# Kernel optimization log

Hardware: AMD Instinct MI355X
Metric: run time of the kernel (lower is better)

The kernel has to match this reference:

```python
import jax, jax.numpy as jnp
import numpy as np

TOKEN_DIM = 4
EPS = 1e-6


def setup_inputs() -> dict:
    key = jax.random.key(0)
    k_x, k_w = jax.random.split(key)
    B, S, E = 8, 8192, 512
    EMB = 512
    x = jax.random.normal(k_x, (B, S, E), dtype=jnp.float32)
    ln_gamma = jnp.ones((E,), dtype=jnp.float32)
    ln_beta = jnp.zeros((E,), dtype=jnp.float32)
    # glorot-ish scale for the compression kernel [token_dim*E, EMB]
    W = jax.random.normal(k_w, (TOKEN_DIM * E, EMB), dtype=jnp.float32) * 0.02
    b = jnp.zeros((EMB,), dtype=jnp.float32)
    return {"x": x, "ln_gamma": ln_gamma, "ln_beta": ln_beta, "W": W, "b": b}


def reference(x, ln_gamma, ln_beta, W, b):
    B, S, E = x.shape
    # LayerNormalization over the feature axis (center + scale)
    mean = jnp.mean(x, axis=-1, keepdims=True)
    var = jnp.mean(jnp.square(x - mean), axis=-1, keepdims=True)
    h = (x - mean) * jax.lax.rsqrt(var + EPS) * ln_gamma + ln_beta
    # Divide: split sequence axis by token_dim and merge factor into feature axis
    # [B, S, E] -> [B, S//T, T*E]
    h = h.reshape(B, S // TOKEN_DIM, TOKEN_DIM * E)
    # Dense compression + exact gelu (keras 'gelu' uses erf form)
    out = jnp.einsum('bsf,fd->bsd', h, W) + b
    return jax.nn.gelu(out, approximate=False)
```

## Files before the change

### kernel.cpp

```cpp
#include <hip/hip_runtime.h>
#include <hip/hip_bf16.h>
#include <cstdint>

#define XROWS   65536
#define E       512
#define MROWS   16384
#define KDIM    2048
#define NDIM    512
#define NT      32

typedef __attribute__((ext_vector_type(4))) float f32x4;
typedef __attribute__((ext_vector_type(8))) unsigned short u16x8;
typedef __attribute__((ext_vector_type(8))) __bf16 bf16x8;

__device__ __forceinline__ unsigned short f2bf(float f) {
  unsigned u = __builtin_bit_cast(unsigned, f);
  u += 0x7FFFu + ((u >> 16) & 1u);
  return (unsigned short)(u >> 16);
}

typedef const __attribute__((address_space(1))) unsigned char ga_u8;
typedef __attribute__((address_space(3))) unsigned char ls_u8;
__device__ __forceinline__ void gload16(const void* g, void* l) {
  __builtin_amdgcn_global_load_lds((ga_u8*)g, (ls_u8*)l, 16, 0, 0);
}

__device__ __forceinline__ float gelu_f(float v) {
  float p = v * (2.3022083f + 0.1029432f * (v * v));
  p = fminf(p, 80.0f);
  const float Ee = exp2f(p);
  return v * Ee * __builtin_amdgcn_rcpf(Ee + 1.0f);
}

__global__ __launch_bounds__(256) void wt_kernel(const float* __restrict__ W,
                                                 const float* __restrict__ gamma,
                                                 unsigned short* __restrict__ WT) {
  __shared__ float tile[64][68];
  const int t  = threadIdx.x;
  const int bk = blockIdx.x >> 3;
  const int bn = blockIdx.x & 7;
  const int c4 = (t & 15) * 4;
#pragma unroll
  for (int i = 0; i < 4; ++i) {
    const int r = (t >> 4) + i * 16;
    const f32x4 v = *(const f32x4*)&W[(size_t)(bk * 64 + r) * NDIM + bn * 64 + c4];
    tile[r][c4 + 0] = v.x; tile[r][c4 + 1] = v.y;
    tile[r][c4 + 2] = v.z; tile[r][c4 + 3] = v.w;
  }
  __syncthreads();
#pragma unroll
  for (int j = 0; j < 2; ++j) {
    const int n  = j * 32 + (t >> 3);
    const int kb = (t & 7) * 8;
    const int kg0 = (bk & 7) * 64 + kb;
    const f32x4 g0 = *(const f32x4*)(gamma + kg0);
    const f32x4 g1 = *(const f32x4*)(gamma + kg0 + 4);
    const float gg[8] = {g0.x, g0.y, g0.z, g0.w, g1.x, g1.y, g1.z, g1.w};
    u16x8 o;
#pragma unroll
    for (int q = 0; q < 8; ++q) o[q] = f2bf(gg[q] * tile[kb + q][n]);
    *(u16x8*)&WT[(size_t)(bn * 64 + n) * KDIM + bk * 64 + kb] = o;
  }
}

__global__ __launch_bounds__(256) void kbias1(const float* __restrict__ W,
                                              const float* __restrict__ beta,
                                              float* __restrict__ partial) {
  const int bk = blockIdx.x, tid = threadIdx.x;
  float a0 = 0.f, a1 = 0.f;
  for (int k = 0; k < 64; ++k) {
    const int kg = bk * 64 + k;
    const float be = beta[kg & (E - 1)];
    a0 += be * W[(size_t)kg * NDIM + tid];
    a1 += be * W[(size_t)kg * NDIM + 256 + tid];
  }
  partial[bk * NDIM + tid] = a0;
  partial[bk * NDIM + 256 + tid] = a1;
}

__global__ __launch_bounds__(256) void kbias2(const float* __restrict__ b,
                                              const float* __restrict__ partial,
                                              float* __restrict__ biasf) {
  const int c = blockIdx.x * 256 + threadIdx.x;
  float s = b[c];
  for (int j = 0; j < 32; ++j) s += partial[j * NDIM + c];
  biasf[c] = s;
}

__global__ __launch_bounds__(256, 4) void ln_kernel(const float* __restrict__ x,
                                                    unsigned short* __restrict__ h) {
  const int w = threadIdx.x >> 6, l = threadIdx.x & 63;
  const size_t row = (size_t)blockIdx.x * 4 + w;
  const float* xr = x + row * E + l * 8;
  const f32x4 v0 = *(const f32x4*)xr;
  const f32x4 v1 = *(const f32x4*)(xr + 4);
  float xv[8] = {v0.x, v0.y, v0.z, v0.w, v1.x, v1.y, v1.z, v1.w};
  float s = 0.f, q = 0.f;
#pragma unroll
  for (int j = 0; j < 8; ++j) { s += xv[j]; q += xv[j] * xv[j]; }
#pragma unroll
  for (int off = 32; off > 0; off >>= 1) {
    s += __shfl_xor(s, off);
    q += __shfl_xor(q, off);
  }
  const float mean = s * (1.0f / E);
  const float var  = q * (1.0f / E) - mean * mean;
  const float rstd = rsqrtf(var + 1e-6f);
  const float nm   = -mean * rstd;
  u16x8 o;
#pragma unroll
  for (int j = 0; j < 8; ++j) o[j] = f2bf(xv[j] * rstd + nm);
  *(u16x8*)(h + row * E + l * 8) = o;
}

__global__ __launch_bounds__(256, 3) void gemm_kernel(const unsigned short* __restrict__ A,
                                                      const unsigned short* __restrict__ Bt,
                                                      const float* __restrict__ biasf,
                                                      float* __restrict__ out) {
  __shared__ char smem[32768];
  const int tid = threadIdx.x;
  const int l = tid & 63, w = tid >> 6;
  const int l7 = l & 7, l15 = l & 15, lhi = l >> 4;
  const int wr = w >> 1, wc = w & 1;

  const int wg = ((blockIdx.x & 7) << 6) | (blockIdx.x >> 3);
  const int bn = wg & 3;
  const int bm = wg >> 2;
  const size_t arow0 = (size_t)bm * 128;
  const int    brow0 = bn * 128;

  const int srow = w * 8 + (l >> 3);
  const int swz  = (l7 * 16) ^ ((l >> 3) << 4);
  const char* gA = (const char*)A  + ((size_t)(arow0 + srow) * KDIM) * 2 + swz;
  const char* gB = (const char*)Bt + ((size_t)(brow0 + srow) * KDIM) * 2 + swz;

  f32x4 acc[4][4];
#pragma unroll
  for (int m = 0; m < 4; ++m)
#pragma unroll
    for (int n = 0; n < 4; ++n) acc[m][n] = (f32x4){0.f, 0.f, 0.f, 0.f};

  const int cs0 = (lhi * 16) ^ (l7 * 16);

  for (int t = 0; t < NT; ++t) {
    __syncthreads();
    {
      const char* pa = gA + (size_t)t * 128;
      const char* pb = gB + (size_t)t * 128;
#pragma unroll
      for (int i = 0; i < 4; ++i) {
        gload16(pa + (size_t)i * 32 * KDIM * 2, smem + (i * 32 + w * 8) * 128);
        gload16(pb + (size_t)i * 32 * KDIM * 2, smem + 16384 + (i * 32 + w * 8) * 128);
      }
    }
    __syncthreads();
#pragma unroll
    for (int kk = 0; kk < 2; ++kk) {
      const int co = cs0 ^ (kk * 64);
      bf16x8 av[4], bv[4];
#pragma unroll
      for (int m = 0; m < 4; ++m)
        av[m] = *(const bf16x8*)(smem + (wr * 64 + m * 16 + l15) * 128 + co);
#pragma unroll
      for (int n = 0; n < 4; ++n)
        bv[n] = *(const bf16x8*)(smem + 16384 + (wc * 64 + n * 16 + l15) * 128 + co);
#pragma unroll
      for (int m = 0; m < 4; ++m)
#pragma unroll
        for (int n = 0; n < 4; ++n)
          acc[m][n] = __builtin_amdgcn_mfma_f32_16x16x32_bf16(av[m], bv[n],
                                                              acc[m][n], 0, 0, 0);
    }
  }

#pragma unroll
  for (int n = 0; n < 4; ++n) {
    const int col = brow0 + wc * 64 + n * 16 + l15;
    const float bb = biasf[col];
#pragma unroll
    for (int m = 0; m < 4; ++m) {
      const size_t rbase = arow0 + wr * 64 + m * 16 + lhi * 4;
#pragma unroll
      for (int r = 0; r < 4; ++r) {
        const float v = acc[m][n][r] + bb;
        out[(rbase + r) * NDIM + col] = gelu_f(v);
      }
    }
  }
}

extern "C" void kernel_launch(void* const* d_in, const int* in_sizes, int n_in,
                              void* d_out, int out_size, void* d_ws, size_t ws_size,
                              hipStream_t stream) {
  const float* x     = (const float*)d_in[0];
  const float* gamma = (const float*)d_in[1];
  const float* beta  = (const float*)d_in[2];
  const float* W     = (const float*)d_in[3];
  const float* b     = (const float*)d_in[4];
  float* out = (float*)d_out;

  char* p = (char*)d_ws;
  unsigned short* WT = (unsigned short*)p;            p += (size_t)NDIM * KDIM * 2;
  unsigned short* h  = (unsigned short*)p;            p += (size_t)MROWS * KDIM * 2;
  float* partial     = (float*)p;                     p += (size_t)32 * NDIM * 4;
  float* biasf       = (float*)p;

  wt_kernel<<<256, 256, 0, stream>>>(W, gamma, WT);
  kbias1<<<32, 256, 0, stream>>>(W, beta, partial);
  kbias2<<<2, 256, 0, stream>>>(b, partial, biasf);
  ln_kernel<<<XROWS / 4, 256, 0, stream>>>(x, h);
  gemm_kernel<<<(MROWS / 128) * 4, 256, 0, stream>>>(h, WT, biasf, out);
}
```

Before: 83.69 us.

## Double-buffer GEMM LDS tiles to overlap global loads with MFMA

The GEMM kernel now uses two LDS buffers and prefetches the next K tile with global_load_lds while computing on the current one. Explicit vmcnt waits and raw barriers replace the double __syncthreads. MFMA sections also get raised wave priority via s_setprio. This hides global load latency, but doubling LDS to 64KB lowers occupancy, so launch bounds drop from 3 to 2 blocks per CU.

```diff
diff --git a/kernel.cpp b/kernel.cpp
--- a/kernel.cpp
+++ b/kernel.cpp
@@ -113,11 +113,13 @@
   *(u16x8*)(h + row * E + l * 8) = o;
 }
 
-__global__ __launch_bounds__(256, 3) void gemm_kernel(const unsigned short* __restrict__ A,
+#define VMCNT(n) asm volatile("s_waitcnt vmcnt(" #n ")" ::: "memory")
+
+__global__ __launch_bounds__(256, 2) void gemm_kernel(const unsigned short* __restrict__ A,
                                                       const unsigned short* __restrict__ Bt,
                                                       const float* __restrict__ biasf,
                                                       float* __restrict__ out) {
-  __shared__ char smem[32768];
+  __shared__ char smem[2 * 32768];
   const int tid = threadIdx.x;
   const int l = tid & 63, w = tid >> 6;
   const int l7 = l & 7, l15 = l & 15, lhi = l >> 4;
@@ -134,6 +136,17 @@
   const char* gA = (const char*)A  + ((size_t)(arow0 + srow) * KDIM) * 2 + swz;
   const char* gB = (const char*)Bt + ((size_t)(brow0 + srow) * KDIM) * 2 + swz;
 
+  auto stage = [&](int t) {
+    char* base = smem + (t & 1) * 32768;
+    const char* pa = gA + (size_t)t * 128;
+    const char* pb = gB + (size_t)t * 128;
+#pragma unroll
+    for (int i = 0; i < 4; ++i) {
+      gload16(pa + (size_t)i * 32 * KDIM * 2, base + (i * 32 + w * 8) * 128);
+      gload16(pb + (size_t)i * 32 * KDIM * 2, base + 16384 + (i * 32 + w * 8) * 128);
+    }
+  };
+
   f32x4 acc[4][4];
 #pragma unroll
   for (int m = 0; m < 4; ++m)
@@ -142,35 +155,40 @@
 
   const int cs0 = (lhi * 16) ^ (l7 * 16);
 
+  stage(0);
+
   for (int t = 0; t < NT; ++t) {
-    __syncthreads();
-    {
-      const char* pa = gA + (size_t)t * 128;
-      const char* pb = gB + (size_t)t * 128;
-#pragma unroll
-      for (int i = 0; i < 4; ++i) {
-        gload16(pa + (size_t)i * 32 * KDIM * 2, smem + (i * 32 + w * 8) * 128);
-        gload16(pb + (size_t)i * 32 * KDIM * 2, smem + 16384 + (i * 32 + w * 8) * 128);
-      }
-    }
-    __syncthreads();
+    if (t + 1 < NT) {
+      stage(t + 1);
+      VMCNT(8);
+    } else {
+      VMCNT(0);
+    }
+    __builtin_amdgcn_s_barrier();
+
+    const char* Ab = smem + (t & 1) * 32768;
+    const char* Bb = Ab + 16384;
 #pragma unroll
     for (int kk = 0; kk < 2; ++kk) {
       const int co = cs0 ^ (kk * 64);
       bf16x8 av[4], bv[4];
 #pragma unroll
       for (int m = 0; m < 4; ++m)
-        av[m] = *(const bf16x8*)(smem + (wr * 64 + m * 16 + l15) * 128 + co);
+        av[m] = *(const bf16x8*)(Ab + (wr * 64 + m * 16 + l15) * 128 + co);
 #pragma unroll
       for (int n = 0; n < 4; ++n)
-        bv[n] = *(const bf16x8*)(smem + 16384 + (wc * 64 + n * 16 + l15) * 128 + co);
+        bv[n] = *(const bf16x8*)(Bb + (wc * 64 + n * 16 + l15) * 128 + co);
+      __builtin_amdgcn_s_setprio(1);
 #pragma unroll
       for (int m = 0; m < 4; ++m)
 #pragma unroll
         for (int n = 0; n < 4; ++n)
           acc[m][n] = __builtin_amdgcn_mfma_f32_16x16x32_bf16(av[m], bv[n],
                                                               acc[m][n], 0, 0, 0);
-    }
+      __builtin_amdgcn_s_setprio(0);
+    }
+    asm volatile("s_waitcnt lgkmcnt(0)" ::: "memory");
+    __builtin_amdgcn_s_barrier();
   }
 
 #pragma unroll
```

Result: no change. 83.92 us (+0.3%).

## Rewrite GEMM as 256x128 tile, 8-wave double-buffered pipeline with split prefetch

Applied to the files above, without the earlier changes.

The GEMM now uses 512-thread blocks on 256x128 output tiles with double-buffered LDS (96KB). Global-to-LDS loads for the next k-step are interleaved across four sub-phases, with explicit vmcnt waits, barriers and setprio around the MFMA bursts. The goal is to overlap memory loads with matrix-core work and raise reuse per tile, replacing the old load-sync-compute loop. The cost is one block per CU, many barriers per iteration, and a fragile manual wait-count schedule.

```diff
diff --git a/kernel.cpp b/kernel.cpp
--- a/kernel.cpp
+++ b/kernel.cpp
@@ -113,73 +113,122 @@
   *(u16x8*)(h + row * E + l * 8) = o;
 }
 
-__global__ __launch_bounds__(256, 3) void gemm_kernel(const unsigned short* __restrict__ A,
+#define VMCNT(n) asm volatile("s_waitcnt vmcnt(" #n ")" ::: "memory")
+#define LGKM0()  asm volatile("s_waitcnt lgkmcnt(0)" ::: "memory")
+
+__global__ __launch_bounds__(512, 1) void gemm_kernel(const unsigned short* __restrict__ A,
                                                       const unsigned short* __restrict__ Bt,
                                                       const float* __restrict__ biasf,
                                                       float* __restrict__ out) {
-  __shared__ char smem[32768];
+  __shared__ char smem[98304];
   const int tid = threadIdx.x;
   const int l = tid & 63, w = tid >> 6;
   const int l7 = l & 7, l15 = l & 15, lhi = l >> 4;
-  const int wr = w >> 1, wc = w & 1;
-
-  const int wg = ((blockIdx.x & 7) << 6) | (blockIdx.x >> 3);
+  const int wr = w >> 2, wc = w & 3;
+
+  const int wg = ((blockIdx.x & 7) << 5) | (blockIdx.x >> 3);
   const int bn = wg & 3;
   const int bm = wg >> 2;
-  const size_t arow0 = (size_t)bm * 128;
-  const int    brow0 = bn * 128;
-
-  const int srow = w * 8 + (l >> 3);
-  const int swz  = (l7 * 16) ^ ((l >> 3) << 4);
+  const size_t arow0 = (size_t)bm * 256;
+  const int    ncol0 = bn * 128;
+
+  const int srow = tid >> 3;
+  const int swz  = ((tid & 7) * 16) ^ ((srow & 7) << 4);
   const char* gA = (const char*)A  + ((size_t)(arow0 + srow) * KDIM) * 2 + swz;
-  const char* gB = (const char*)Bt + ((size_t)(brow0 + srow) * KDIM) * 2 + swz;
-
-  f32x4 acc[4][4];
-#pragma unroll
-  for (int m = 0; m < 4; ++m)
-#pragma unroll
-    for (int n = 0; n < 4; ++n) acc[m][n] = (f32x4){0.f, 0.f, 0.f, 0.f};
+  const char* gB = (const char*)Bt + ((size_t)(ncol0 + srow) * KDIM) * 2 + swz;
+
+  auto stageA = [&](int t, int h, int mh) {
+    gload16(gA + ((size_t)(h * 128 + mh * 64) * KDIM) * 2 + (size_t)t * 128,
+            smem + (t & 1) * 32768 + h * 16384 + (mh * 64 + w * 8) * 128);
+  };
+  auto stageB = [&](int t, int c) {
+    gload16(gB + ((size_t)(c * 64) * KDIM) * 2 + (size_t)t * 128,
+            smem + 65536 + (t & 1) * 16384 + (c * 64 + w * 8) * 128);
+  };
+
+  f32x4 acc[8][2];
+#pragma unroll
+  for (int m = 0; m < 8; ++m) {
+    acc[m][0] = (f32x4){0.f, 0.f, 0.f, 0.f};
+    acc[m][1] = (f32x4){0.f, 0.f, 0.f, 0.f};
+  }
 
   const int cs0 = (lhi * 16) ^ (l7 * 16);
 
-  for (int t = 0; t < NT; ++t) {
-    __syncthreads();
-    {
-      const char* pa = gA + (size_t)t * 128;
-      const char* pb = gB + (size_t)t * 128;
-#pragma unroll
-      for (int i = 0; i < 4; ++i) {
-        gload16(pa + (size_t)i * 32 * KDIM * 2, smem + (i * 32 + w * 8) * 128);
-        gload16(pb + (size_t)i * 32 * KDIM * 2, smem + 16384 + (i * 32 + w * 8) * 128);
-      }
-    }
-    __syncthreads();
-#pragma unroll
-    for (int kk = 0; kk < 2; ++kk) {
-      const int co = cs0 ^ (kk * 64);
-      bf16x8 av[4], bv[4];
-#pragma unroll
-      for (int m = 0; m < 4; ++m)
-        av[m] = *(const bf16x8*)(smem + (wr * 64 + m * 16 + l15) * 128 + co);
-#pragma unroll
-      for (int n = 0; n < 4; ++n)
-        bv[n] = *(const bf16x8*)(smem + 16384 + (wc * 64 + n * 16 + l15) * 128 + co);
-#pragma unroll
-      for (int m = 0; m < 4; ++m)
-#pragma unroll
-        for (int n = 0; n < 4; ++n)
-          acc[m][n] = __builtin_amdgcn_mfma_f32_16x16x32_bf16(av[m], bv[n],
-                                                              acc[m][n], 0, 0, 0);
-    }
-  }
-
-#pragma unroll
-  for (int n = 0; n < 4; ++n) {
-    const int col = brow0 + wc * 64 + n * 16 + l15;
+#define DS_LOADS(p, mh, kk)                                                     \
+  const char* Ab = smem + (p) * 32768 + wr * 16384;                             \
+  const char* Bb = smem + 65536 + (p) * 16384;                                  \
+  const int co = cs0 ^ ((kk) * 64);                                             \
+  bf16x8 a0 = *(const bf16x8*)(Ab + ((mh) * 64 +  0 + l15) * 128 + co);         \
+  bf16x8 a1 = *(const bf16x8*)(Ab + ((mh) * 64 + 16 + l15) * 128 + co);         \
+  bf16x8 a2 = *(const bf16x8*)(Ab + ((mh) * 64 + 32 + l15) * 128 + co);         \
+  bf16x8 a3 = *(const bf16x8*)(Ab + ((mh) * 64 + 48 + l15) * 128 + co);         \
+  bf16x8 b0 = *(const bf16x8*)(Bb + (wc * 32 +  0 + l15) * 128 + co);           \
+  bf16x8 b1 = *(const bf16x8*)(Bb + (wc * 32 + 16 + l15) * 128 + co)
+
+#define MFMA8(mh)                                                               \
+  acc[(mh)*4+0][0] = __builtin_amdgcn_mfma_f32_16x16x32_bf16(a0, b0, acc[(mh)*4+0][0], 0,0,0); \
+  acc[(mh)*4+0][1] = __builtin_amdgcn_mfma_f32_16x16x32_bf16(a0, b1, acc[(mh)*4+0][1], 0,0,0); \
+  acc[(mh)*4+1][0] = __builtin_amdgcn_mfma_f32_16x16x32_bf16(a1, b0, acc[(mh)*4+1][0], 0,0,0); \
+  acc[(mh)*4+1][1] = __builtin_amdgcn_mfma_f32_16x16x32_bf16(a1, b1, acc[(mh)*4+1][1], 0,0,0); \
+  acc[(mh)*4+2][0] = __builtin_amdgcn_mfma_f32_16x16x32_bf16(a2, b0, acc[(mh)*4+2][0], 0,0,0); \
+  acc[(mh)*4+2][1] = __builtin_amdgcn_mfma_f32_16x16x32_bf16(a2, b1, acc[(mh)*4+2][1], 0,0,0); \
+  acc[(mh)*4+3][0] = __builtin_amdgcn_mfma_f32_16x16x32_bf16(a3, b0, acc[(mh)*4+3][0], 0,0,0); \
+  acc[(mh)*4+3][1] = __builtin_amdgcn_mfma_f32_16x16x32_bf16(a3, b1, acc[(mh)*4+3][1], 0,0,0)
+
+  stageA(0, 0, 0); stageA(0, 1, 0);
+  stageA(0, 0, 1); stageA(0, 1, 1);
+  stageB(0, 0);    stageB(0, 1);
+  stageA(1, 0, 0); stageA(1, 1, 0);
+  VMCNT(2);
+  __builtin_amdgcn_s_barrier();
+
+  for (int tau = 0; tau < NT; ++tau) {
+    const int p = tau & 1;
+    {
+      DS_LOADS(p, 0, 0);
+      if (tau + 1 < NT) { stageB(tau + 1, 0); stageB(tau + 1, 1); }
+      __builtin_amdgcn_s_barrier();
+      LGKM0(); __builtin_amdgcn_sched_barrier(0);
+      __builtin_amdgcn_s_setprio(1); MFMA8(0); __builtin_amdgcn_s_setprio(0);
+      __builtin_amdgcn_s_barrier();
+    }
+    {
+      DS_LOADS(p, 0, 1);
+      if (tau + 1 < NT) { stageA(tau + 1, 0, 1); stageA(tau + 1, 1, 1); }
+      __builtin_amdgcn_s_barrier();
+      LGKM0(); __builtin_amdgcn_sched_barrier(0);
+      __builtin_amdgcn_s_setprio(1); MFMA8(0); __builtin_amdgcn_s_setprio(0);
+      __builtin_amdgcn_s_barrier();
+    }
+    {
+      DS_LOADS(p, 1, 0);
+      if (tau + 2 < NT) { stageA(tau + 2, 0, 0); stageA(tau + 2, 1, 0); }
+      __builtin_amdgcn_s_barrier();
+      LGKM0(); __builtin_amdgcn_sched_barrier(0);
+      __builtin_amdgcn_s_setprio(1); MFMA8(1); __builtin_amdgcn_s_setprio(0);
+      __builtin_amdgcn_s_barrier();
+    }
+    {
+      DS_LOADS(p, 1, 1);
+      __builtin_amdgcn_s_barrier();
+      LGKM0(); __builtin_amdgcn_sched_barrier(0);
+      __builtin_amdgcn_s_setprio(1); MFMA8(1); __builtin_amdgcn_s_setprio(0);
+      if (tau + 2 < NT)      VMCNT(2);
+      else if (tau + 1 < NT) VMCNT(0);
+      __builtin_amdgcn_s_barrier();
+    }
+  }
+#undef DS_LOADS
+#undef MFMA8
+
+#pragma unroll
+  for (int n = 0; n < 2; ++n) {
+    const int col = ncol0 + wc * 32 + n * 16 + l15;
     const float bb = biasf[col];
 #pragma unroll
-    for (int m = 0; m < 4; ++m) {
-      const size_t rbase = arow0 + wr * 64 + m * 16 + lhi * 4;
+    for (int m = 0; m < 8; ++m) {
+      const size_t rbase = arow0 + wr * 128 + m * 16 + lhi * 4;
 #pragma unroll
       for (int r = 0; r < 4; ++r) {
         const float v = acc[m][n][r] + bb;
@@ -209,5 +258,5 @@
   kbias1<<<32, 256, 0, stream>>>(W, beta, partial);
   kbias2<<<2, 256, 0, stream>>>(b, partial, biasf);
   ln_kernel<<<XROWS / 4, 256, 0, stream>>>(x, h);
-  gemm_kernel<<<(MROWS / 128) * 4, 256, 0, stream>>>(h, WT, biasf, out);
-}
+  gemm_kernel<<<(MROWS / 256) * 4, 512, 0, stream>>>(h, WT, biasf, out);
+}
```

After: 85.87 us. 2.6% more time.
